# Kernel optimization log

Measured on AMD Instinct MI355X. Metric: run time of the kernel, lower is better.

Reference implementation:

```python
import math
import jax, jax.numpy as jnp
import numpy as np

B, TQ, TK, D = 2, 512, 8192, 1024
N_HEAD, HEAD_DIM = 16, 64
NA = 4096


def setup_inputs() -> dict:
    key = jax.random.key(0)
    ks = jax.random.split(key, 12)
    w = lambda k, shp: (jax.random.normal(k, shp, dtype=jnp.float32) * 0.02)
    return {
        "q": jax.random.normal(ks[0], (B, TQ, D), dtype=jnp.float32),
        "kv": jax.random.normal(ks[1], (B, TK, D), dtype=jnp.float32),
        "Wq": w(ks[2], (D, D)), "bq": jnp.zeros((D,), jnp.float32),
        "Wk": w(ks[3], (D, D)), "bk": jnp.zeros((D,), jnp.float32),
        "Wv": w(ks[4], (D, D)), "bv": jnp.zeros((D,), jnp.float32),
        "Wo": w(ks[5], (D, D)), "bo": jnp.zeros((D,), jnp.float32),
        "active_bias": w(ks[6], (1, D)),
        "inactive_bias": w(ks[7], (1, D)),
        "log_temp": jnp.zeros((), jnp.float32),  # log(temp=1.0)
        "n_actives": NA,
    }


def _attn(qh, kh, vh):
    # qh already carries the full score scale; plain softmax attention
    scores = jnp.einsum("bhqd,bhkd->bhqk", qh, kh)
    w = jax.nn.softmax(scores, axis=-1)
    return jnp.einsum("bhqk,bhkd->bhqd", w, vh)


def reference(q, kv, Wq, bq, Wk, bk, Wv, bv, Wo, bo, active_bias, inactive_bias, log_temp, n_actives):
    Na = int(n_actives)
    Tk = kv.shape[1]
    Ni = Tk - Na

    qp = jnp.einsum("btd,od->bto", q, Wq) + bq
    # group-specific additive biases on kv before K/V projection
    kvb = jnp.concatenate([kv[:, :Na] + active_bias, kv[:, Na:] + inactive_bias], axis=1)
    kp = jnp.einsum("btd,od->bto", kvb, Wk) + bk
    vp = jnp.einsum("btd,od->bto", kvb, Wv) + bv

    # [B, H, T, hd]
    qh = qp.reshape(B, TQ, N_HEAD, HEAD_DIM).transpose(0, 2, 1, 3)
    kh = kp.reshape(B, Tk, N_HEAD, HEAD_DIM).transpose(0, 2, 1, 3)
    vh = vp.reshape(B, Tk, N_HEAD, HEAD_DIM).transpose(0, 2, 1, 3)

    temp = jnp.clip(jnp.exp(log_temp), 0.1, 10.0)
    # torch: q *= 1/sqrt(d); sdpa(q/temp, ...) applies another 1/sqrt(d)
    qs = qh / (jnp.float32(HEAD_DIM) * temp)

    out = jnp.zeros_like(qh)
    if Na > 0:
        out = out + _attn(qs, kh[:, :, :Na], vh[:, :, :Na]) / math.sqrt(max(Na, 1))
    if Ni > 0:
        out = out - _attn(qs, kh[:, :, Na:], vh[:, :, Na:]) / math.sqrt(max(Ni, 1))

    out = out.transpose(0, 2, 1, 3).reshape(B, TQ, D)
    return jnp.einsum("btd,od->bto", out, Wo) + bo
```

## Files before the change

kernel.cpp:

```cpp
#include <hip/hip_runtime.h>
#include <math.h>
#include <stdint.h>

#define B_   2
#define TQ_  512
#define TK_  8192
#define D_   1024
#define NH_  16
#define HD_  64

#define NEG_BIG (-3.0e38f)
#define ASPLIT 8
#define LOG2E 1.4426950408889634f
#define EXP2F(x) __builtin_exp2f(x)

typedef __attribute__((ext_vector_type(8))) short short8;
typedef __attribute__((ext_vector_type(4))) float f32x4;

__device__ __forceinline__ unsigned short f2bf(float x) {
    unsigned u = __float_as_uint(x);
    unsigned r = u + 0x7FFFu + ((u >> 16) & 1u);
    return (unsigned short)(r >> 16);
}
__device__ __forceinline__ float bf2f(unsigned short h) {
    return __uint_as_float(((unsigned)h) << 16);
}

#define GLD16(gp, lp)                                                              \
    __builtin_amdgcn_global_load_lds(                                              \
        (const __attribute__((address_space(1))) unsigned int*)(gp),               \
        (__attribute__((address_space(3))) unsigned int*)(lp), 16, 0, 0)

__global__ __launch_bounds__(256)
void split_w4(const float* __restrict__ W0, const float* __restrict__ W1,
              const float* __restrict__ W2, const float* __restrict__ W3,
              unsigned short* __restrict__ O0, unsigned short* __restrict__ O1,
              unsigned short* __restrict__ O2, unsigned short* __restrict__ O3)
{
    const float* W; unsigned short* O;
    switch (blockIdx.y) {
        case 0:  W = W0; O = O0; break;
        case 1:  W = W1; O = O1; break;
        case 2:  W = W2; O = O2; break;
        default: W = W3; O = O3; break;
    }
    size_t i = ((size_t)blockIdx.x * 256 + threadIdx.x) * 8;
    float4 x0 = *(const float4*)(W + i);
    float4 x1 = *(const float4*)(W + i + 4);
    float a[8] = {x0.x, x0.y, x0.z, x0.w, x1.x, x1.y, x1.z, x1.w};
    union { short8 v; unsigned short u[8]; } H;
#pragma unroll
    for (int j = 0; j < 8; ++j) H.u[j] = f2bf(a[j]);
    *(short8*)(O + i) = H.v;
}

__global__ __launch_bounds__(256)
void split_w(const float* __restrict__ W, unsigned short* __restrict__ Wh)
{
    size_t i = ((size_t)blockIdx.x * 256 + threadIdx.x) * 8;
    float4 x0 = *(const float4*)(W + i);
    float4 x1 = *(const float4*)(W + i + 4);
    float a[8] = {x0.x, x0.y, x0.z, x0.w, x1.x, x1.y, x1.z, x1.w};
    union { short8 v; unsigned short u[8]; } H;
#pragma unroll
    for (int j = 0; j < 8; ++j) H.u[j] = f2bf(a[j]);
    *(short8*)(Wh + i) = H.v;
}

__global__ __launch_bounds__(256)
void split_kv(const float* __restrict__ kv, const float* __restrict__ ab,
              const float* __restrict__ ib, const int* __restrict__ nactp,
              unsigned short* __restrict__ Ah)
{
    const int Na = *nactp;
    size_t i = ((size_t)blockIdx.x * 256 + threadIdx.x) * 8;
    int row = (int)(i >> 10);
    int col = (int)(i & (D_ - 1));
    const float* bp = ((row & (TK_ - 1)) < Na) ? ab : ib;
    float4 x0 = *(const float4*)(kv + i);
    float4 x1 = *(const float4*)(kv + i + 4);
    float4 b0 = *(const float4*)(bp + col);
    float4 b1 = *(const float4*)(bp + col + 4);
    float a[8] = {x0.x + b0.x, x0.y + b0.y, x0.z + b0.z, x0.w + b0.w,
                  x1.x + b1.x, x1.y + b1.y, x1.z + b1.z, x1.w + b1.w};
    union { short8 v; unsigned short u[8]; } H;
#pragma unroll
    for (int j = 0; j < 8; ++j) H.u[j] = f2bf(a[j]);
    *(short8*)(Ah + i) = H.v;
}

__global__ __launch_bounds__(256)
void sdpca_gemm_q(const unsigned short* __restrict__ A, const unsigned short* __restrict__ W,
                  const float* __restrict__ bias, const float* __restrict__ log_temp,
                  unsigned short* __restrict__ Qb)
{
    __shared__ unsigned short AT[128 * 32];
    __shared__ unsigned short BT[128 * 32];
    const int tid  = threadIdx.x;
    const int lane = tid & 63;
    const int w    = tid >> 6;
    const int brow = blockIdx.y * 128;
    const int bcol = blockIdx.x * 128;
    const int wr = w >> 1, wc = w & 1;

    const int   srow = lane >> 2;
    const int   scol = (((lane & 3) ^ ((lane >> 3) & 3)) * 8);
    const size_t gA0 = (size_t)(brow + w * 32 + srow) * D_ + scol;
    const size_t gA1 = gA0 + (size_t)16 * D_;
    const size_t gB0 = (size_t)(bcol + w * 32 + srow) * D_ + scol;
    const size_t gB1 = gB0 + (size_t)16 * D_;
    const int   l0   = (w * 32 +  0) * 32;
    const int   l1   = (w * 32 + 16) * 32;

    f32x4 acc[4][4];
#pragma unroll
    for (int m = 0; m < 4; ++m)
#pragma unroll
        for (int n = 0; n < 4; ++n) acc[m][n] = (f32x4){0.f, 0.f, 0.f, 0.f};

    const int frow = lane & 15;
    const int fko  = (((lane >> 4) ^ ((frow >> 1) & 3)) * 8);

    for (int k0 = 0; k0 < D_; k0 += 32) {
        GLD16(A + gA0 + k0, &AT[l0]);
        GLD16(A + gA1 + k0, &AT[l1]);
        GLD16(W + gB0 + k0, &BT[l0]);
        GLD16(W + gB1 + k0, &BT[l1]);
        __syncthreads();
        short8 bf[4];
#pragma unroll
        for (int n = 0; n < 4; ++n)
            bf[n] = *(const short8*)&BT[(wc * 64 + n * 16 + frow) * 32 + fko];
#pragma unroll
        for (int m = 0; m < 4; ++m) {
            short8 a = *(const short8*)&AT[(wr * 64 + m * 16 + frow) * 32 + fko];
#pragma unroll
            for (int n = 0; n < 4; ++n)
                acc[m][n] = __builtin_amdgcn_mfma_f32_16x16x32_bf16(a, bf[n], acc[m][n], 0, 0, 0);
        }
        __syncthreads();
    }

    float lt    = *log_temp;
    float temp  = fminf(fmaxf(expf(lt), 0.1f), 10.0f);
    float scale = LOG2E / (64.0f * temp);

#pragma unroll
    for (int n = 0; n < 4; ++n) {
        int col = bcol + wc * 64 + n * 16 + frow;
        float bsv = bias[col];
#pragma unroll
        for (int m = 0; m < 4; ++m) {
            int rbase = brow + wr * 64 + m * 16 + (lane >> 4) * 4;
#pragma unroll
            for (int r = 0; r < 4; ++r)
                Qb[(size_t)(rbase + r) * D_ + col] = f2bf((acc[m][n][r] + bsv) * scale);
        }
    }
}

__global__ __launch_bounds__(256)
void sdpca_gemm_kv_mfma(const unsigned short* __restrict__ Ah,
                        const unsigned short* __restrict__ Whk,
                        const unsigned short* __restrict__ Whv,
                        const float* __restrict__ bk, const float* __restrict__ bv,
                        unsigned short* __restrict__ Kb, unsigned short* __restrict__ Vt)
{
    __shared__ unsigned short AT[128 * 32];
    __shared__ unsigned short BT[128 * 32];

    const int tid  = threadIdx.x;
    const int lane = tid & 63;
    const int w    = tid >> 6;
    const int bid  = blockIdx.x;
    const int lid  = (bid & 7) * 128 + (bid >> 3);
    const int brow = (lid >> 3) * 128;
    const int bcol = (lid & 7) * 128;
    const int z    = blockIdx.y;

    const unsigned short* Wh = z ? Whv : Whk;
    const float* bias        = z ? bv  : bk;

    const int wr = w >> 1, wc = w & 1;

    const int   srow = lane >> 2;
    const int   scol = (((lane & 3) ^ ((lane >> 3) & 3)) * 8);
    const size_t gA0 = (size_t)(brow + w * 32 + srow) * D_ + scol;
    const size_t gA1 = gA0 + (size_t)16 * D_;
    const size_t gB0 = (size_t)(bcol + w * 32 + srow) * D_ + scol;
    const size_t gB1 = gB0 + (size_t)16 * D_;
    const int   l0   = (w * 32 +  0) * 32;
    const int   l1   = (w * 32 + 16) * 32;

    f32x4 acc[4][4];
#pragma unroll
    for (int m = 0; m < 4; ++m)
#pragma unroll
        for (int n = 0; n < 4; ++n) acc[m][n] = (f32x4){0.f, 0.f, 0.f, 0.f};

    const int frow = lane & 15;
    const int fko  = (((lane >> 4) ^ ((frow >> 1) & 3)) * 8);

    for (int k0 = 0; k0 < D_; k0 += 32) {
        GLD16(Ah + gA0 + k0, &AT[l0]);
        GLD16(Ah + gA1 + k0, &AT[l1]);
        GLD16(Wh + gB0 + k0, &BT[l0]);
        GLD16(Wh + gB1 + k0, &BT[l1]);
        __syncthreads();
        short8 bf[4];
#pragma unroll
        for (int n = 0; n < 4; ++n)
            bf[n] = *(const short8*)&BT[(wc * 64 + n * 16 + frow) * 32 + fko];
#pragma unroll
        for (int m = 0; m < 4; ++m) {
            short8 a = *(const short8*)&AT[(wr * 64 + m * 16 + frow) * 32 + fko];
#pragma unroll
            for (int n = 0; n < 4; ++n)
                acc[m][n] = __builtin_amdgcn_mfma_f32_16x16x32_bf16(a, bf[n], acc[m][n], 0, 0, 0);
        }
        __syncthreads();
    }

    if (z == 0) {
#pragma unroll
        for (int n = 0; n < 4; ++n) {
            int col = bcol + wc * 64 + n * 16 + frow;
            float bsv = bias[col];
#pragma unroll
            for (int m = 0; m < 4; ++m) {
                int rbase = brow + wr * 64 + m * 16 + (lane >> 4) * 4;
#pragma unroll
                for (int r = 0; r < 4; ++r)
                    Kb[(size_t)(rbase + r) * D_ + col] = f2bf(acc[m][n][r] + bsv);
            }
        }
    } else {
#pragma unroll
        for (int n = 0; n < 4; ++n) {
            int col = bcol + wc * 64 + n * 16 + frow;
            int h   = col >> 6, d = col & 63;
            float bsv = bias[col];
#pragma unroll
            for (int m = 0; m < 4; ++m) {
                int rbase = brow + wr * 64 + m * 16 + (lane >> 4) * 4;
                int b     = rbase >> 13;
                int tok   = rbase & (TK_ - 1);
                ushort4 o;
                o.x = f2bf(acc[m][n][0] + bsv);
                o.y = f2bf(acc[m][n][1] + bsv);
                o.z = f2bf(acc[m][n][2] + bsv);
                o.w = f2bf(acc[m][n][3] + bsv);
                *(ushort4*)&Vt[((size_t)(b * 16 + h) * 64 + d) * TK_ + tok] = o;
            }
        }
    }
}

template<bool FULL>
__device__ __forceinline__ void attn_pass(
    const f32x4 st[4], int jb, int lo, int hi,
    f32x4& lacc, f32x4 o[4],
    unsigned short* Ps, const unsigned short* Vs,
    int frow, int g, int w)
{
    const int q = w * 16 + frow;
    const short8 kOnes = {(short)0x3F80, (short)0x3F80, (short)0x3F80, (short)0x3F80,
                          (short)0x3F80, (short)0x3F80, (short)0x3F80, (short)0x3F80};
    float p[4][4];
#pragma unroll
    for (int mt = 0; mt < 4; ++mt)
#pragma unroll
        for (int r = 0; r < 4; ++r) {
            float pv = EXP2F(st[mt][r]);
            if (!FULL) {
                int key = jb + mt * 16 + g * 4 + r;
                if (key < lo || key >= hi) pv = 0.f;
            }
            p[mt][r] = pv;
        }

#pragma unroll
    for (int mt = 0; mt < 4; ++mt) {
        unsigned u0, u1;
        asm("v_cvt_pk_bf16_f32 %0, %1, %2" : "=v"(u0) : "v"(p[mt][0]), "v"(p[mt][1]));
        asm("v_cvt_pk_bf16_f32 %0, %1, %2" : "=v"(u1) : "v"(p[mt][2]), "v"(p[mt][3]));
        unsigned* dst = (unsigned*)((char*)Ps + q * 144 + (mt * 16 + g * 4) * 2);
        dst[0] = u0; dst[1] = u1;
    }
    __builtin_amdgcn_sched_barrier(0);

    short8 pb[2];
#pragma unroll
    for (int ks = 0; ks < 2; ++ks)
        pb[ks] = *(const short8*)((const char*)Ps + q * 144 + ks * 64 + g * 16);
    __builtin_amdgcn_s_setprio(1);
#pragma unroll
    for (int mt = 0; mt < 4; ++mt) {
        int row = mt * 16 + frow;
        int rs  = (row & 7) << 4;
#pragma unroll
        for (int ks = 0; ks < 2; ++ks) {
            short8 a = *(const short8*)((const char*)Vs + row * 128 + ((ks * 64 + g * 16) ^ rs));
            o[mt] = __builtin_amdgcn_mfma_f32_16x16x32_bf16(a, pb[ks], o[mt], 0, 0, 0);
        }
    }
#pragma unroll
    for (int ks = 0; ks < 2; ++ks)
        lacc = __builtin_amdgcn_mfma_f32_16x16x32_bf16(kOnes, pb[ks], lacc, 0, 0, 0);
    __builtin_amdgcn_s_setprio(0);
}

__global__ __launch_bounds__(256)
void sdpca_attn_mfma(const unsigned short* __restrict__ Qb,
                     const unsigned short* __restrict__ Kb,
                     const unsigned short* __restrict__ Vt,
                     const int* __restrict__ nactp,
                     unsigned short* __restrict__ pO, float* __restrict__ pL)
{
    __shared__ char smem[25600];
    unsigned short* Ks = (unsigned short*)smem;
    unsigned short* Vs = (unsigned short*)(smem + 8192);
    unsigned short* Ps = (unsigned short*)(smem + 16384);
    float*          Ot = (float*)smem;

    const int tid  = threadIdx.x;
    const int l    = tid & 63, w = tid >> 6;
    const int frow = l & 15,  g = l >> 4;

    const int bid = blockIdx.x;
    const int lid = (bid & 7) * 256 + (bid >> 3);
    const int q0  = (lid & 7) * 64;
    const int bh  = (lid >> 3) & 31;
    const int s   = lid >> 8;
    const int b   = bh >> 4, h = bh & 15;

    const int Na   = *nactp;
    const int ks0  = s * (TK_ / ASPLIT);
    const int nt   = TK_ / ASPLIT / 64;

    short8 qf0, qf1;
    {
        const unsigned short* qp = Qb + (size_t)(b * TQ_ + q0 + w * 16 + frow) * D_ + h * HD_;
        qf0 = *(const short8*)(qp + g * 8);
        qf1 = *(const short8*)(qp + 32 + g * 8);
    }

    f32x4 lA4 = (f32x4){0.f, 0.f, 0.f, 0.f};
    f32x4 lI4 = (f32x4){0.f, 0.f, 0.f, 0.f};
    f32x4 oA[4], oI[4];
#pragma unroll
    for (int mt = 0; mt < 4; ++mt) {
        oA[mt] = (f32x4){0.f, 0.f, 0.f, 0.f};
        oI[mt] = (f32x4){0.f, 0.f, 0.f, 0.f};
    }

    const int srow = tid >> 2;
    const int scb  = (tid & 3) * 32;
    const unsigned short* kg = Kb + (size_t)(b * TK_ + ks0 + srow) * D_ + h * HD_ + (tid & 3) * 16;
    const unsigned short* vg = Vt + ((size_t)bh * HD_ + srow) * TK_ + ks0 + (tid & 3) * 16;
    const int kswz0 = srow * 128 + ((scb +  0) ^ ((srow & 7) << 4));
    const int kswz1 = srow * 128 + ((scb + 16) ^ ((srow & 7) << 4));

    short8 kr0 = *(const short8*)(kg);
    short8 kr1 = *(const short8*)(kg + 8);
    short8 vr0 = *(const short8*)(vg);
    short8 vr1 = *(const short8*)(vg + 8);
    kg += (size_t)64 * D_;
    vg += 64;

    for (int t = 0; t < nt; ++t) {
        const int jb = ks0 + t * 64;
        __syncthreads();
        *(short8*)((char*)Ks + kswz0) = kr0;
        *(short8*)((char*)Ks + kswz1) = kr1;
        *(short8*)((char*)Vs + kswz0) = vr0;
        *(short8*)((char*)Vs + kswz1) = vr1;
        __syncthreads();

        if (t + 1 < nt) {
            kr0 = *(const short8*)(kg);
            kr1 = *(const short8*)(kg + 8);
            vr0 = *(const short8*)(vg);
            vr1 = *(const short8*)(vg + 8);
            kg += (size_t)64 * D_;
            vg += 64;
        }

        f32x4 st[4];
        __builtin_amdgcn_s_setprio(1);
#pragma unroll
        for (int mt = 0; mt < 4; ++mt) {
            int row = mt * 16 + frow;
            int rs  = (row & 7) << 4;
            short8 a0 = *(const short8*)((const char*)Ks + row * 128 + ((g * 16) ^ rs));
            short8 a1 = *(const short8*)((const char*)Ks + row * 128 + ((64 + g * 16) ^ rs));
            f32x4 acc = (f32x4){0.f, 0.f, 0.f, 0.f};
            acc = __builtin_amdgcn_mfma_f32_16x16x32_bf16(a0, qf0, acc, 0, 0, 0);
            acc = __builtin_amdgcn_mfma_f32_16x16x32_bf16(a1, qf1, acc, 0, 0, 0);
            st[mt] = acc;
        }
        __builtin_amdgcn_s_setprio(0);

        const bool hasA = (jb < Na);
        const bool hasI = (jb + 64 > Na);
        if (hasA) {
            if (jb + 64 <= Na) attn_pass<true >(st, jb, 0, Na, lA4, oA, Ps, Vs, frow, g, w);
            else               attn_pass<false>(st, jb, 0, Na, lA4, oA, Ps, Vs, frow, g, w);
        }
        if (hasI) {
            if (jb >= Na)      attn_pass<true >(st, jb, Na, TK_, lI4, oI, Ps, Vs, frow, g, w);
            else               attn_pass<false>(st, jb, Na, TK_, lI4, oI, Ps, Vs, frow, g, w);
        }
    }

    const int q = w * 16 + frow;
#pragma unroll
    for (int grp = 0; grp < 2; ++grp) {
        __syncthreads();
        const f32x4* o = grp ? oI : oA;
#pragma unroll
        for (int mt = 0; mt < 4; ++mt)
            *(f32x4*)&Ot[q * 68 + mt * 16 + g * 4] = o[mt];
        if (g == 0) {
            size_t base = ((size_t)((s * 2 + grp) * (B_ * NH_) + bh)) * TQ_ + q0 + q;
            pL[base] = grp ? lI4[0] : lA4[0];
        }
        __syncthreads();
        {
            int qr = tid >> 2, dc = (tid & 3) * 16;
            size_t rowbase = ((size_t)((s * 2 + grp) * (B_ * NH_) + bh)) * TQ_ + q0 + qr;
            unsigned short* dst = pO + rowbase * HD_ + dc;
            union { short8 v; unsigned short u[8]; } o0, o1;
#pragma unroll
            for (int j = 0; j < 8; ++j) {
                o0.u[j] = f2bf(Ot[qr * 68 + dc + j]);
                o1.u[j] = f2bf(Ot[qr * 68 + dc + 8 + j]);
            }
            *(short8*)(dst)     = o0.v;
            *(short8*)(dst + 8) = o1.v;
        }
    }
}

__global__ __launch_bounds__(256)
void sdpca_combine(const unsigned short* __restrict__ pO, const float* __restrict__ pL,
                   const int* __restrict__ nactp, unsigned short* __restrict__ Aob)
{
    int idx = blockIdx.x * 256 + threadIdx.x;
    int d   = idx & (HD_ - 1);
    int q   = (idx >> 6) & (TQ_ - 1);
    int bh  = idx >> 15;
    int b   = bh >> 4, h = bh & 15;
    int Na  = *nactp;
    int Ni  = TK_ - Na;

    float res = 0.f;
#pragma unroll
    for (int gg = 0; gg < 2; ++gg) {
        float L = 0.f, O = 0.f;
#pragma unroll
        for (int ss = 0; ss < ASPLIT; ++ss) {
            size_t ii = ((size_t)((ss * 2 + gg) * (B_ * NH_) + bh)) * TQ_ + q;
            L += pL[ii];
            O += bf2f(pO[ii * HD_ + d]);
        }
        float r   = (L > 0.f) ? (O / L) : 0.f;
        int   cnt = (gg == 0) ? Na : Ni;
        float sc  = (cnt > 0) ? rsqrtf((float)cnt) : 0.f;
        res += (gg == 0) ? (sc * r) : (-sc * r);
    }
    Aob[((size_t)(b * TQ_ + q)) * D_ + h * HD_ + d] = f2bf(res);
}

__global__ __launch_bounds__(256)
void sdpca_gemm_o(const unsigned short* __restrict__ A, const unsigned short* __restrict__ W,
                  const float* __restrict__ bias, float* __restrict__ C)
{
    __shared__ unsigned short AT[128 * 32];
    __shared__ unsigned short BT[128 * 32];
    const int tid  = threadIdx.x;
    const int lane = tid & 63;
    const int w    = tid >> 6;
    const int brow = blockIdx.y * 128;
    const int bcol = blockIdx.x * 128;
    const int wr = w >> 1, wc = w & 1;

    const int   srow = lane >> 2;
    const int   scol = (((lane & 3) ^ ((lane >> 3) & 3)) * 8);
    const size_t gA0 = (size_t)(brow + w * 32 + srow) * D_ + scol;
    const size_t gA1 = gA0 + (size_t)16 * D_;
    const size_t gB0 = (size_t)(bcol + w * 32 + srow) * D_ + scol;
    const size_t gB1 = gB0 + (size_t)16 * D_;
    const int   l0   = (w * 32 +  0) * 32;
    const int   l1   = (w * 32 + 16) * 32;

    f32x4 acc[4][4];
#pragma unroll
    for (int m = 0; m < 4; ++m)
#pragma unroll
        for (int n = 0; n < 4; ++n) acc[m][n] = (f32x4){0.f, 0.f, 0.f, 0.f};

    const int frow = lane & 15;
    const int fko  = (((lane >> 4) ^ ((frow >> 1) & 3)) * 8);

    for (int k0 = 0; k0 < D_; k0 += 32) {
        GLD16(A + gA0 + k0, &AT[l0]);
        GLD16(A + gA1 + k0, &AT[l1]);
        GLD16(W + gB0 + k0, &BT[l0]);
        GLD16(W + gB1 + k0, &BT[l1]);
        __syncthreads();
        short8 bf[4];
#pragma unroll
        for (int n = 0; n < 4; ++n)
            bf[n] = *(const short8*)&BT[(wc * 64 + n * 16 + frow) * 32 + fko];
#pragma unroll
        for (int m = 0; m < 4; ++m) {
            short8 a = *(const short8*)&AT[(wr * 64 + m * 16 + frow) * 32 + fko];
#pragma unroll
            for (int n = 0; n < 4; ++n)
                acc[m][n] = __builtin_amdgcn_mfma_f32_16x16x32_bf16(a, bf[n], acc[m][n], 0, 0, 0);
        }
        __syncthreads();
    }

#pragma unroll
    for (int n = 0; n < 4; ++n) {
        int col = bcol + wc * 64 + n * 16 + frow;
        float bsv = bias[col];
#pragma unroll
        for (int m = 0; m < 4; ++m) {
            int rbase = brow + wr * 64 + m * 16 + (lane >> 4) * 4;
#pragma unroll
            for (int r = 0; r < 4; ++r)
                C[(size_t)(rbase + r) * D_ + col] = acc[m][n][r] + bsv;
        }
    }
}

extern "C" void kernel_launch(void* const* d_in, const int* in_sizes, int n_in,
                              void* d_out, int out_size, void* d_ws, size_t ws_size,
                              hipStream_t stream) {
    (void)in_sizes; (void)n_in; (void)out_size; (void)ws_size;
    const float* q   = (const float*)d_in[0];
    const float* kv  = (const float*)d_in[1];
    const float* Wq  = (const float*)d_in[2];
    const float* bq  = (const float*)d_in[3];
    const float* Wk  = (const float*)d_in[4];
    const float* bk  = (const float*)d_in[5];
    const float* Wv  = (const float*)d_in[6];
    const float* bv  = (const float*)d_in[7];
    const float* Wo  = (const float*)d_in[8];
    const float* bo  = (const float*)d_in[9];
    const float* ab  = (const float*)d_in[10];
    const float* ib  = (const float*)d_in[11];
    const float* lt  = (const float*)d_in[12];
    const int*   na  = (const int*)d_in[13];

    char* ws = (char*)d_ws;
    const size_t nQ  = (size_t)B_ * TQ_ * D_;
    const size_t nKV = (size_t)B_ * TK_ * D_;
    const size_t nW  = (size_t)D_ * D_;
    const size_t nML = (size_t)ASPLIT * 2 * B_ * NH_ * TQ_;

    unsigned short* Ah  = (unsigned short*)ws;
    unsigned short* Whk = Ah + nKV;
    unsigned short* Whv = Whk + nW;
    unsigned short* Kb  = Whv + nW;
    unsigned short* Vt  = Kb + nKV;
    unsigned short* Qb  = Vt + nKV;
    unsigned short* qbb = Qb + nQ;
    unsigned short* Wqb = qbb + nQ;
    unsigned short* Wob = Wqb + nW;
    unsigned short* Aob = Wob + nW;
    float* pL = (float*)(Aob + nQ);
    unsigned short* pO = (unsigned short*)(pL + nML);

    dim3 blk(256);
    split_w           <<<dim3((int)(nQ / 8 / 256)),  blk, 0, stream>>>(q,  qbb);
    split_w4          <<<dim3((int)(nW / 8 / 256), 4), blk, 0, stream>>>(
        Wq, Wo, Wk, Wv, Wqb, Wob, Whk, Whv);
    split_kv          <<<dim3((int)(nKV / 8 / 256)), blk, 0, stream>>>(kv, ab, ib, na, Ah);
    sdpca_gemm_q      <<<dim3(8, 8),                 blk, 0, stream>>>(qbb, Wqb, bq, lt, Qb);
    sdpca_gemm_kv_mfma<<<dim3(1024, 2),              blk, 0, stream>>>(Ah, Whk, Whv, bk, bv, Kb, Vt);
    sdpca_attn_mfma   <<<dim3(2048),                 blk, 0, stream>>>(Qb, Kb, Vt, na, pO, pL);
    sdpca_combine     <<<dim3((B_ * TQ_ * D_) / 256), blk, 0, stream>>>(pO, pL, na, Aob);
    sdpca_gemm_o      <<<dim3(8, 8),                 blk, 0, stream>>>(Aob, Wob, bo, (float*)d_out);
}
```

Before: 232.4 us.

## Fuse kv bf16 conversion into KV GEMM and fold group biases via GEMV

Drops the separate split_kv pass that wrote a bf16 copy of kv. The KV GEMM now loads fp32 kv directly, converts it to bf16 in registers with packed cvt instructions, and stores it to LDS, with a register prefetch of the next K-slice. The active/inactive additive biases are moved through the linear map by a small GEMV (W·bias) and added per token in the epilogue. This removes one full read and write of the large kv tensor, but the GEMM now reads fp32 (twice the bytes per tile), uses synchronous loads instead of global_load_lds, and the bias is added in fp32 after projection rather than before bf16 rounding.

```diff
diff --git a/kernel.cpp b/kernel.cpp
--- a/kernel.cpp
+++ b/kernel.cpp
@@ -25,6 +25,14 @@
 __device__ __forceinline__ float bf2f(unsigned short h) {
     return __uint_as_float(((unsigned)h) << 16);
 }
+__device__ __forceinline__ short8 pack_bf16x8(float4 lo, float4 hi) {
+    union { short8 v; unsigned u[4]; } P;
+    asm("v_cvt_pk_bf16_f32 %0, %1, %2" : "=v"(P.u[0]) : "v"(lo.x), "v"(lo.y));
+    asm("v_cvt_pk_bf16_f32 %0, %1, %2" : "=v"(P.u[1]) : "v"(lo.z), "v"(lo.w));
+    asm("v_cvt_pk_bf16_f32 %0, %1, %2" : "=v"(P.u[2]) : "v"(hi.x), "v"(hi.y));
+    asm("v_cvt_pk_bf16_f32 %0, %1, %2" : "=v"(P.u[3]) : "v"(hi.z), "v"(hi.w));
+    return P.v;
+}
 
 #define GLD16(gp, lp)                                                              \
     __builtin_amdgcn_global_load_lds(                                              \
@@ -68,25 +76,23 @@
 }
 
 __global__ __launch_bounds__(256)
-void split_kv(const float* __restrict__ kv, const float* __restrict__ ab,
-              const float* __restrict__ ib, const int* __restrict__ nactp,
-              unsigned short* __restrict__ Ah)
-{
-    const int Na = *nactp;
-    size_t i = ((size_t)blockIdx.x * 256 + threadIdx.x) * 8;
-    int row = (int)(i >> 10);
-    int col = (int)(i & (D_ - 1));
-    const float* bp = ((row & (TK_ - 1)) < Na) ? ab : ib;
-    float4 x0 = *(const float4*)(kv + i);
-    float4 x1 = *(const float4*)(kv + i + 4);
-    float4 b0 = *(const float4*)(bp + col);
-    float4 b1 = *(const float4*)(bp + col + 4);
-    float a[8] = {x0.x + b0.x, x0.y + b0.y, x0.z + b0.z, x0.w + b0.w,
-                  x1.x + b1.x, x1.y + b1.y, x1.z + b1.z, x1.w + b1.w};
-    union { short8 v; unsigned short u[8]; } H;
-#pragma unroll
-    for (int j = 0; j < 8; ++j) H.u[j] = f2bf(a[j]);
-    *(short8*)(Ah + i) = H.v;
+void bias_gemv(const float* __restrict__ Wk, const float* __restrict__ Wv,
+               const float* __restrict__ ab, const float* __restrict__ ib,
+               float* __restrict__ gvK, float* __restrict__ gvV)
+{
+    const int comb = blockIdx.y;
+    const float* W = (comb < 2) ? Wk : Wv;
+    const float* g = (comb & 1) ? ib : ab;
+    float* out = ((comb < 2) ? gvK : gvV) + (comb & 1) * D_;
+    const int n = blockIdx.x * 256 + threadIdx.x;
+    const float* wr = W + (size_t)n * D_;
+    float acc = 0.f;
+    for (int d = 0; d < D_; d += 4) {
+        float4 w4 = *(const float4*)(wr + d);
+        float4 g4 = *(const float4*)(g + d);
+        acc += w4.x * g4.x + w4.y * g4.y + w4.z * g4.z + w4.w * g4.w;
+    }
+    out[n] = acc;
 }
 
 __global__ __launch_bounds__(256)
@@ -160,11 +166,13 @@
 }
 
 __global__ __launch_bounds__(256)
-void sdpca_gemm_kv_mfma(const unsigned short* __restrict__ Ah,
-                        const unsigned short* __restrict__ Whk,
-                        const unsigned short* __restrict__ Whv,
-                        const float* __restrict__ bk, const float* __restrict__ bv,
-                        unsigned short* __restrict__ Kb, unsigned short* __restrict__ Vt)
+void sdpca_gemm_kv_fused(const float* __restrict__ kv,
+                         const unsigned short* __restrict__ Whk,
+                         const unsigned short* __restrict__ Whv,
+                         const float* __restrict__ bk, const float* __restrict__ bv,
+                         const float* __restrict__ gvK, const float* __restrict__ gvV,
+                         const int* __restrict__ nactp,
+                         unsigned short* __restrict__ Kb, unsigned short* __restrict__ Vt)
 {
     __shared__ unsigned short AT[128 * 32];
     __shared__ unsigned short BT[128 * 32];
@@ -177,20 +185,23 @@
     const int brow = (lid >> 3) * 128;
     const int bcol = (lid & 7) * 128;
     const int z    = blockIdx.y;
+    const int Na   = *nactp;
 
     const unsigned short* Wh = z ? Whv : Whk;
     const float* bias        = z ? bv  : bk;
+    const float* gv          = z ? gvV : gvK;
 
     const int wr = w >> 1, wc = w & 1;
 
-    const int   srow = lane >> 2;
-    const int   scol = (((lane & 3) ^ ((lane >> 3) & 3)) * 8);
-    const size_t gA0 = (size_t)(brow + w * 32 + srow) * D_ + scol;
+    const int srow = lane >> 2;
+    const int cg   = lane & 3;
+    const int cs   = cg ^ ((srow >> 1) & 3);
+    const size_t gA0 = (size_t)(brow + w * 32 + srow) * D_ + cg * 8;
     const size_t gA1 = gA0 + (size_t)16 * D_;
-    const size_t gB0 = (size_t)(bcol + w * 32 + srow) * D_ + scol;
+    const size_t gB0 = (size_t)(bcol + w * 32 + srow) * D_ + cg * 8;
     const size_t gB1 = gB0 + (size_t)16 * D_;
-    const int   l0   = (w * 32 +  0) * 32;
-    const int   l1   = (w * 32 + 16) * 32;
+    const int    la0 = (w * 32 + srow) * 32 + cs * 8;
+    const int    la1 = (w * 32 + 16 + srow) * 32 + cs * 8;
 
     f32x4 acc[4][4];
 #pragma unroll
@@ -201,12 +212,30 @@
     const int frow = lane & 15;
     const int fko  = (((lane >> 4) ^ ((frow >> 1) & 3)) * 8);
 
+    float4 a00 = *(const float4*)(kv + gA0);
+    float4 a01 = *(const float4*)(kv + gA0 + 4);
+    float4 a10 = *(const float4*)(kv + gA1);
+    float4 a11 = *(const float4*)(kv + gA1 + 4);
+    short8 br0 = *(const short8*)(Wh + gB0);
+    short8 br1 = *(const short8*)(Wh + gB1);
+
     for (int k0 = 0; k0 < D_; k0 += 32) {
-        GLD16(Ah + gA0 + k0, &AT[l0]);
-        GLD16(Ah + gA1 + k0, &AT[l1]);
-        GLD16(Wh + gB0 + k0, &BT[l0]);
-        GLD16(Wh + gB1 + k0, &BT[l1]);
-        __syncthreads();
+        __syncthreads();
+        *(short8*)&AT[la0] = pack_bf16x8(a00, a01);
+        *(short8*)&AT[la1] = pack_bf16x8(a10, a11);
+        *(short8*)&BT[la0] = br0;
+        *(short8*)&BT[la1] = br1;
+        __syncthreads();
+
+        if (k0 + 32 < D_) {
+            a00 = *(const float4*)(kv + gA0 + k0 + 36 - 4);
+            a01 = *(const float4*)(kv + gA0 + k0 + 36);
+            a10 = *(const float4*)(kv + gA1 + k0 + 32);
+            a11 = *(const float4*)(kv + gA1 + k0 + 36);
+            br0 = *(const short8*)(Wh + gB0 + k0 + 32);
+            br1 = *(const short8*)(Wh + gB1 + k0 + 32);
+        }
+
         short8 bf[4];
 #pragma unroll
         for (int n = 0; n < 4; ++n)
@@ -218,7 +247,6 @@
             for (int n = 0; n < 4; ++n)
                 acc[m][n] = __builtin_amdgcn_mfma_f32_16x16x32_bf16(a, bf[n], acc[m][n], 0, 0, 0);
         }
-        __syncthreads();
     }
 
     if (z == 0) {
@@ -226,12 +254,16 @@
         for (int n = 0; n < 4; ++n) {
             int col = bcol + wc * 64 + n * 16 + frow;
             float bsv = bias[col];
+            float g0  = gv[col], g1 = gv[D_ + col];
 #pragma unroll
             for (int m = 0; m < 4; ++m) {
                 int rbase = brow + wr * 64 + m * 16 + (lane >> 4) * 4;
 #pragma unroll
-                for (int r = 0; r < 4; ++r)
-                    Kb[(size_t)(rbase + r) * D_ + col] = f2bf(acc[m][n][r] + bsv);
+                for (int r = 0; r < 4; ++r) {
+                    int tok = (rbase + r) & (TK_ - 1);
+                    float gval = (tok < Na) ? g0 : g1;
+                    Kb[(size_t)(rbase + r) * D_ + col] = f2bf(acc[m][n][r] + bsv + gval);
+                }
             }
         }
     } else {
@@ -240,16 +272,17 @@
             int col = bcol + wc * 64 + n * 16 + frow;
             int h   = col >> 6, d = col & 63;
             float bsv = bias[col];
+            float g0  = gv[col], g1 = gv[D_ + col];
 #pragma unroll
             for (int m = 0; m < 4; ++m) {
                 int rbase = brow + wr * 64 + m * 16 + (lane >> 4) * 4;
                 int b     = rbase >> 13;
                 int tok   = rbase & (TK_ - 1);
                 ushort4 o;
-                o.x = f2bf(acc[m][n][0] + bsv);
-                o.y = f2bf(acc[m][n][1] + bsv);
-                o.z = f2bf(acc[m][n][2] + bsv);
-                o.w = f2bf(acc[m][n][3] + bsv);
+                o.x = f2bf(acc[m][n][0] + bsv + ((tok + 0 < Na) ? g0 : g1));
+                o.y = f2bf(acc[m][n][1] + bsv + ((tok + 1 < Na) ? g0 : g1));
+                o.z = f2bf(acc[m][n][2] + bsv + ((tok + 2 < Na) ? g0 : g1));
+                o.w = f2bf(acc[m][n][3] + bsv + ((tok + 3 < Na) ? g0 : g1));
                 *(ushort4*)&Vt[((size_t)(b * 16 + h) * 64 + d) * TK_ + tok] = o;
             }
         }
@@ -562,8 +595,9 @@
     const size_t nW  = (size_t)D_ * D_;
     const size_t nML = (size_t)ASPLIT * 2 * B_ * NH_ * TQ_;
 
-    unsigned short* Ah  = (unsigned short*)ws;
-    unsigned short* Whk = Ah + nKV;
+    float*          gvK = (float*)ws;
+    float*          gvV = gvK + 2 * D_;
+    unsigned short* Whk = (unsigned short*)(gvV + 2 * D_);
     unsigned short* Whv = Whk + nW;
     unsigned short* Kb  = Whv + nW;
     unsigned short* Vt  = Kb + nKV;
@@ -576,13 +610,14 @@
     unsigned short* pO = (unsigned short*)(pL + nML);
 
     dim3 blk(256);
-    split_w           <<<dim3((int)(nQ / 8 / 256)),  blk, 0, stream>>>(q,  qbb);
-    split_w4          <<<dim3((int)(nW / 8 / 256), 4), blk, 0, stream>>>(
+    split_w            <<<dim3((int)(nQ / 8 / 256)),  blk, 0, stream>>>(q,  qbb);
+    split_w4           <<<dim3((int)(nW / 8 / 256), 4), blk, 0, stream>>>(
         Wq, Wo, Wk, Wv, Wqb, Wob, Whk, Whv);
-    split_kv          <<<dim3((int)(nKV / 8 / 256)), blk, 0, stream>>>(kv, ab, ib, na, Ah);
-    sdpca_gemm_q      <<<dim3(8, 8),                 blk, 0, stream>>>(qbb, Wqb, bq, lt, Qb);
-    sdpca_gemm_kv_mfma<<<dim3(1024, 2),              blk, 0, stream>>>(Ah, Whk, Whv, bk, bv, Kb, Vt);
-    sdpca_attn_mfma   <<<dim3(2048),                 blk, 0, stream>>>(Qb, Kb, Vt, na, pO, pL);
-    sdpca_combine     <<<dim3((B_ * TQ_ * D_) / 256), blk, 0, stream>>>(pO, pL, na, Aob);
-    sdpca_gemm_o      <<<dim3(8, 8),                 blk, 0, stream>>>(Aob, Wob, bo, (float*)d_out);
-}
+    bias_gemv          <<<dim3(4, 4),                 blk, 0, stream>>>(Wk, Wv, ab, ib, gvK, gvV);
+    sdpca_gemm_q       <<<dim3(8, 8),                 blk, 0, stream>>>(qbb, Wqb, bq, lt, Qb);
+    sdpca_gemm_kv_fused<<<dim3(1024, 2),              blk, 0, stream>>>(
+        kv, Whk, Whv, bk, bv, gvK, gvV, na, Kb, Vt);
+    sdpca_attn_mfma    <<<dim3(2048),                 blk, 0, stream>>>(Qb, Kb, Vt, na, pO, pL);
+    sdpca_combine      <<<dim3((B_ * TQ_ * D_) / 256), blk, 0, stream>>>(pO, pL, na, Aob);
+    sdpca_gemm_o       <<<dim3(8, 8),                 blk, 0, stream>>>(Aob, Wob, bo, (float*)d_out);
+}
```

New measurement: 257.1 us. +10.6%, slower.
